# Kernel optimization log

Hardware: AMD Instinct MI355X
Metric: run time of the kernel (lower is better)

The kernel has to match this reference:

```python
import jax, jax.numpy as jnp
from jax import lax
import numpy as np

B, Z, Y, X = 2, 41, 400, 352   # KITTI-like sparse grid
N_TOTAL = 400000               # total active voxels (all batches)
C = 16                         # 16 * SCALING_RATIO channels in stage 1
K = 27                         # 3x3x3 kernel offsets
BN_EPS = 1e-3


def _build_rulebook(rng):
    """Random unique active voxels + [27,N] submanifold neighbor table (-1 = missing)."""
    per_b = N_TOTAL // B
    coords = []
    for b in range(B):
        flat = rng.choice(Z * Y * X, size=per_b, replace=False)
        z, r = np.divmod(flat, Y * X)
        y, x = np.divmod(r, X)
        coords.append(np.stack([np.full(per_b, b), z, y, x], axis=1))
    coords = np.concatenate(coords, 0).astype(np.int32)  # [N,4]
    # padded dense lookup: grid coord -> global voxel row, -1 if inactive
    lut = np.full((B, Z + 2, Y + 2, X + 2), -1, dtype=np.int32)
    lut[coords[:, 0], coords[:, 1] + 1, coords[:, 2] + 1, coords[:, 3] + 1] = np.arange(N_TOTAL, dtype=np.int32)
    offs = [(dz, dy, dx) for dz in (-1, 0, 1) for dy in (-1, 0, 1) for dx in (-1, 0, 1)]
    nbr = np.empty((K, N_TOTAL), dtype=np.int32)
    for k, (dz, dy, dx) in enumerate(offs):
        nbr[k] = lut[coords[:, 0], coords[:, 1] + 1 + dz, coords[:, 2] + 1 + dy, coords[:, 3] + 1 + dx]
    return nbr


def setup_inputs() -> dict:
    key = jax.random.key(0)
    kf, kw0, kw1, kg = jax.random.split(key, 4)
    rng = np.random.default_rng(0)
    nbr = jnp.asarray(_build_rulebook(rng))                      # [27, N] int32
    voxel_features = jax.random.normal(kf, (N_TOTAL, C), jnp.float32)
    w_in = jax.random.normal(kw0, (K, C, C), jnp.float32) * 0.05  # conv_input weight
    g_in = jnp.ones((C,), jnp.float32)
    b_in = jnp.zeros((C,), jnp.float32)
    # 2 SparseBasicBlocks x 2 convs each
    wb = jax.random.normal(kw1, (2, 2, K, C, C), jnp.float32) * 0.05
    gs = jnp.ones((2, 2, C), jnp.float32)
    bs = jnp.zeros((2, 2, C), jnp.float32)
    return {"voxel_features": voxel_features, "nbr": nbr, "w_in": w_in,
            "g_in": g_in, "b_in": b_in, "wb": wb, "gs": gs, "bs": bs}


def _subm_conv(feats, nbr, W):
    """Submanifold 3x3x3 conv: gather active neighbors, GEMM per offset, accumulate.
    feats [N,Cin], nbr [27,N] int32 (-1 = inactive), W [27,Cin,Cout] -> [N,Cout]."""
    out0 = jnp.zeros((feats.shape[0], W.shape[-1]), feats.dtype)
    def body(acc, kw):
        idx, Wk = kw
        valid = idx >= 0
        g = jnp.where(valid[:, None], feats[jnp.where(valid, idx, 0)], 0.0)
        return acc + g @ Wk, None
    acc, _ = lax.scan(body, out0, (nbr, W))
    return acc


def _bn(x, gamma, beta):
    # train-mode BatchNorm1d over voxel dim (biased var, eps=1e-3)
    m = x.mean(0)
    v = x.var(0)
    return (x - m) * lax.rsqrt(v + BN_EPS) * gamma + beta


def reference(voxel_features, nbr, w_in, g_in, b_in, wb, gs, bs):
    # conv_input: SubMConv3d -> BN -> ReLU
    x = jax.nn.relu(_bn(_subm_conv(voxel_features, nbr, w_in), g_in, b_in))
    # conv1: two SparseBasicBlocks sharing the 'subm1' rulebook
    for i in range(2):
        identity = x
        o = jax.nn.relu(_bn(_subm_conv(x, nbr, wb[i, 0]), gs[i, 0], bs[i, 0]))
        o = _bn(_subm_conv(o, nbr, wb[i, 1]), gs[i, 1], bs[i, 1])
        x = jax.nn.relu(o + identity)
    return x
```

## Files before the change

### kernel.cpp

```cpp
#include <hip/hip_runtime.h>

#define N_TOT  400000
#define NTILE  25000
#define NELEM  (N_TOT * 16)
#define CBLK   512
#define GSTRIDE (CBLK * 4)

typedef __attribute__((ext_vector_type(8))) short short8;
typedef __attribute__((ext_vector_type(4))) float f32x4;
typedef __attribute__((ext_vector_type(4))) unsigned short us4;

__device__ __forceinline__ unsigned short f2bf(float x) {
    unsigned int u = __float_as_uint(x);
    u += 0x7FFFu + ((u >> 16) & 1u);
    return (unsigned short)(u >> 16);
}
__device__ __forceinline__ float bf2f(unsigned short h) {
    return __uint_as_float(((unsigned int)h) << 16);
}

__global__ __launch_bounds__(64) void wfrag_k(const float* __restrict__ w_in,
                                              const float* __restrict__ wbs,
                                              unsigned short* __restrict__ wfrag,
                                              unsigned short* __restrict__ xb,
                                              unsigned short* __restrict__ ob) {
    if (blockIdx.x == 0 && threadIdx.x < 8) {
        us4 z = {0, 0, 0, 0};
        unsigned short* base = (threadIdx.x < 4) ? xb : ob;
        reinterpret_cast<us4*>(base + NELEM)[threadIdx.x & 3] = z;
    }
    int b = blockIdx.x;
    int L = b / 14, p = b % 14;
    int l = threadIdx.x;
    int g = l >> 4, col = l & 15;
    int k = 2 * p + (g >> 1);
    int cib = (g & 1) * 8;
    unsigned short v[8];
#pragma unroll
    for (int j = 0; j < 8; ++j) {
        float w = 0.f;
        if (k < 27) {
            int ci = cib + j;
            w = (L == 0) ? w_in[(k * 16 + ci) * 16 + col]
                         : wbs[(((L - 1) * 27 + k) * 16 + ci) * 16 + col];
        }
        v[j] = f2bf(w);
    }
    unsigned short* dst = wfrag + (size_t)(b * 64 + l) * 8;
#pragma unroll
    for (int j = 0; j < 8; ++j) dst[j] = v[j];
}

__global__ __launch_bounds__(256) void cvt_k(const float* __restrict__ in,
                                             unsigned short* __restrict__ out) {
    int i = (blockIdx.x * 256 + threadIdx.x) * 8;
    f32x4 a = *reinterpret_cast<const f32x4*>(in + i);
    f32x4 b = *reinterpret_cast<const f32x4*>(in + i + 4);
    short8 o = { (short)f2bf(a[0]), (short)f2bf(a[1]), (short)f2bf(a[2]), (short)f2bf(a[3]),
                 (short)f2bf(b[0]), (short)f2bf(b[1]), (short)f2bf(b[2]), (short)f2bf(b[3]) };
    *reinterpret_cast<short8*>(out + i) = o;
}

#define IDX(I, tt)                                                              \
  {                                                                             \
    const int vv = (tt) * 16;                                                   \
    _Pragma("unroll")                                                           \
    for (int p = 0; p < 14; ++p) {                                              \
      int k = 2 * p + ksel;                                                     \
      if (k == 13)      I[p] = vv + rc;                                         \
      else if (k < 27)  I[p] = nbr[(size_t)k * N_TOT + vv + rc];                \
      else              I[p] = -1;                                              \
    }                                                                           \
  }

#define GAT(A, I)                                                               \
  {                                                                             \
    _Pragma("unroll")                                                           \
    for (int p = 0; p < 14; ++p) {                                              \
      int ci = I[p] < 0 ? N_TOT : I[p];                                         \
      A[p] = *reinterpret_cast<const short8*>(feats + ((size_t)ci << 4) + half);\
    }                                                                           \
  }

#define CMP(A, tt)                                                              \
  {                                                                             \
    f32x4 acc = {0.f, 0.f, 0.f, 0.f};                                           \
    _Pragma("unroll")                                                           \
    for (int p = 0; p < 14; ++p) {                                              \
      short8 bf = *reinterpret_cast<const short8*>(&wlds[(p * 64 + lane) * 8]); \
      acc = __builtin_amdgcn_mfma_f32_16x16x32_bf16(A[p], bf, acc, 0, 0, 0);    \
    }                                                                           \
    const int vv = (tt) * 16;                                                   \
    _Pragma("unroll")                                                           \
    for (int i = 0; i < 4; ++i)                                                 \
      raw[(size_t)(vv + g * 4 + i) * 16 + rc] = f2bf(acc[i]);                   \
    s_acc += acc[0] + acc[1] + acc[2] + acc[3];                                 \
    q_acc += acc[0]*acc[0] + acc[1]*acc[1] + acc[2]*acc[2] + acc[3]*acc[3];     \
  }

__global__ __launch_bounds__(256, 2) void conv_k(const unsigned short* __restrict__ feats,
                                                 const int* __restrict__ nbr,
                                                 const unsigned short* __restrict__ wfrag,
                                                 unsigned short* __restrict__ raw,
                                                 float* __restrict__ partials) {
    __shared__ unsigned short wlds[14 * 64 * 8];
    __shared__ float red[128];

    {
        const f32x4* src = reinterpret_cast<const f32x4*>(wfrag);
        f32x4* dst = reinterpret_cast<f32x4*>(wlds);
        for (int j = threadIdx.x; j < 896; j += 256) dst[j] = src[j];
    }
    __syncthreads();

    const int lane = threadIdx.x & 63;
    const int wv   = threadIdx.x >> 6;
    const int g    = lane >> 4;
    const int rc   = lane & 15;
    const int half = (g & 1) * 8;
    const int ksel = g >> 1;

    float s_acc = 0.f, q_acc = 0.f;

    int I0[14], I1[14];
    short8 A0[14], A1[14];

    int t0 = blockIdx.x * 4 + wv;
    IDX(I0, t0);
    GAT(A0, I0);
    int t1 = t0 + GSTRIDE;
    if (t1 < NTILE) IDX(I1, t1);

    for (;;) {
        int t2 = t0 + 2 * GSTRIDE;
        if (t2 < NTILE) IDX(I0, t2);
        if (t1 < NTILE) GAT(A1, I1);
        __builtin_amdgcn_sched_barrier(0);
        CMP(A0, t0);
        if (t1 >= NTILE) break;

        int t3 = t1 + 2 * GSTRIDE;
        if (t3 < NTILE) IDX(I1, t3);
        if (t2 < NTILE) GAT(A0, I0);
        __builtin_amdgcn_sched_barrier(0);
        CMP(A1, t1);
        if (t2 >= NTILE) break;

        t0 = t2;
        t1 = t2 + GSTRIDE;
    }

    s_acc += __shfl_xor(s_acc, 16);  s_acc += __shfl_xor(s_acc, 32);
    q_acc += __shfl_xor(q_acc, 16);  q_acc += __shfl_xor(q_acc, 32);
    if (lane < 16) {
        red[wv * 32 + rc]      = s_acc;
        red[wv * 32 + 16 + rc] = q_acc;
    }
    __syncthreads();
    if (threadIdx.x < 32) {
        float v = red[threadIdx.x] + red[32 + threadIdx.x] +
                  red[64 + threadIdx.x] + red[96 + threadIdx.x];
        partials[(size_t)threadIdx.x * CBLK + blockIdx.x] = v;
    }
}

__global__ __launch_bounds__(256) void reduce_k(const float* __restrict__ partials,
                                                float* __restrict__ S) {
    int c = blockIdx.x;
    float s = 0.f;
    for (int i = threadIdx.x; i < CBLK; i += 256) s += partials[(size_t)c * CBLK + i];
    __shared__ float red[256];
    red[threadIdx.x] = s;
    __syncthreads();
#pragma unroll
    for (int off = 128; off > 0; off >>= 1) {
        if (threadIdx.x < off) red[threadIdx.x] += red[threadIdx.x + off];
        __syncthreads();
    }
    if (threadIdx.x == 0) S[c] = red[0];
}

__global__ __launch_bounds__(256) void apply_k(const unsigned short* __restrict__ raw,
                                               const float* __restrict__ S,
                                               const float* __restrict__ gamma,
                                               const float* __restrict__ beta,
                                               const unsigned short* residb,
                                               unsigned short* bfout,
                                               float* f32out) {
    int i = (blockIdx.x * 256 + threadIdx.x) * 8;
    int c0 = i & 8;
    short8 r8 = *reinterpret_cast<const short8*>(raw + i);
    float res[8] = {0, 0, 0, 0, 0, 0, 0, 0};
    if (residb) {
        short8 x8 = *reinterpret_cast<const short8*>(residb + i);
#pragma unroll
        for (int j = 0; j < 8; ++j) res[j] = bf2f((unsigned short)x8[j]);
    }
    const float inv = 1.0f / (float)N_TOT;
    float val[8];
#pragma unroll
    for (int j = 0; j < 8; ++j) {
        int c = c0 + j;
        float m   = S[c] * inv;
        float var = S[16 + c] * inv - m * m;
        float sc  = gamma[c] * rsqrtf(var + 1e-3f);
        float sh  = beta[c] - m * sc;
        val[j] = fmaxf(bf2f((unsigned short)r8[j]) * sc + sh + res[j], 0.f);
    }
    if (bfout) {
        short8 o = { (short)f2bf(val[0]), (short)f2bf(val[1]), (short)f2bf(val[2]), (short)f2bf(val[3]),
                     (short)f2bf(val[4]), (short)f2bf(val[5]), (short)f2bf(val[6]), (short)f2bf(val[7]) };
        *reinterpret_cast<short8*>(bfout + i) = o;
    }
    if (f32out) {
        f32x4 lo = { val[0], val[1], val[2], val[3] };
        f32x4 hi = { val[4], val[5], val[6], val[7] };
        *reinterpret_cast<f32x4*>(f32out + i)     = lo;
        *reinterpret_cast<f32x4*>(f32out + i + 4) = hi;
    }
}

extern "C" void kernel_launch(void* const* d_in, const int* in_sizes, int n_in,
                              void* d_out, int out_size, void* d_ws, size_t ws_size,
                              hipStream_t stream) {
    const float* vf   = (const float*)d_in[0];
    const int*   nbr  = (const int*)  d_in[1];
    const float* w_in = (const float*)d_in[2];
    const float* g_in = (const float*)d_in[3];
    const float* b_in = (const float*)d_in[4];
    const float* wbs  = (const float*)d_in[5];
    const float* gs   = (const float*)d_in[6];
    const float* bs   = (const float*)d_in[7];
    float* out = (float*)d_out;

    char* ws = (char*)d_ws;
    size_t off = 0;
    auto alloc = [&](size_t b) { char* p = ws + off; off += (b + 255) & ~(size_t)255; return p; };
    unsigned short* wfrag = (unsigned short*)alloc((size_t)5 * 14 * 64 * 8 * 2);
    unsigned short* xb    = (unsigned short*)alloc((size_t)(NELEM + 16) * 2);
    unsigned short* ob    = (unsigned short*)alloc((size_t)(NELEM + 16) * 2);
    unsigned short* rb    = (unsigned short*)alloc((size_t)NELEM * 2);
    float*          part  = (float*)alloc((size_t)32 * CBLK * 4);
    float*          S     = (float*)alloc(32 * 4);

    const int FR = 14 * 64 * 8;

    wfrag_k<<<70, 64, 0, stream>>>(w_in, wbs, wfrag, xb, ob);
    cvt_k<<<3125, 256, 0, stream>>>(vf, xb);

    conv_k<<<CBLK, 256, 0, stream>>>(xb, nbr, wfrag, rb, part);
    reduce_k<<<32, 256, 0, stream>>>(part, S);
    apply_k<<<3125, 256, 0, stream>>>(rb, S, g_in, b_in, nullptr, xb, nullptr);

    conv_k<<<CBLK, 256, 0, stream>>>(xb, nbr, wfrag + FR, rb, part);
    reduce_k<<<32, 256, 0, stream>>>(part, S);
    apply_k<<<3125, 256, 0, stream>>>(rb, S, gs + 0, bs + 0, nullptr, ob, nullptr);

    conv_k<<<CBLK, 256, 0, stream>>>(ob, nbr, wfrag + 2 * FR, rb, part);
    reduce_k<<<32, 256, 0, stream>>>(part, S);
    apply_k<<<3125, 256, 0, stream>>>(rb, S, gs + 16, bs + 16, xb, xb, nullptr);

    conv_k<<<CBLK, 256, 0, stream>>>(xb, nbr, wfrag + 3 * FR, rb, part);
    reduce_k<<<32, 256, 0, stream>>>(part, S);
    apply_k<<<3125, 256, 0, stream>>>(rb, S, gs + 32, bs + 32, nullptr, ob, nullptr);

    conv_k<<<CBLK, 256, 0, stream>>>(ob, nbr, wfrag + 4 * FR, rb, part);
    reduce_k<<<32, 256, 0, stream>>>(part, S);
    apply_k<<<3125, 256, 0, stream>>>(rb, S, gs + 48, bs + 48, xb, nullptr, out);
}
```

Baseline: 177.8 us.

## Deepen conv gather pipeline to three stages with predicated neighbor loads

The conv kernel's software pipeline goes from double to triple buffering, so index loads run three tiles ahead and feature gathers two tiles ahead of the MFMA compute. Neighbor-table loads are marked nontemporal, and missing neighbors are now zero-filled by a predicated load instead of reading a zero padding row. The zero-padding rows and their initialization are removed. The aim is to hide more gather latency, at the cost of more registers per thread, which may spill or lower occupancy under launch_bounds(256,2).

```diff
diff --git a/kernel.cpp b/kernel.cpp
--- a/kernel.cpp
+++ b/kernel.cpp
@@ -4,7 +4,7 @@
 #define NTILE  25000
 #define NELEM  (N_TOT * 16)
 #define CBLK   512
-#define GSTRIDE (CBLK * 4)
+#define GS     (CBLK * 4)
 
 typedef __attribute__((ext_vector_type(8))) short short8;
 typedef __attribute__((ext_vector_type(4))) float f32x4;
@@ -21,14 +21,7 @@
 
 __global__ __launch_bounds__(64) void wfrag_k(const float* __restrict__ w_in,
                                               const float* __restrict__ wbs,
-                                              unsigned short* __restrict__ wfrag,
-                                              unsigned short* __restrict__ xb,
-                                              unsigned short* __restrict__ ob) {
-    if (blockIdx.x == 0 && threadIdx.x < 8) {
-        us4 z = {0, 0, 0, 0};
-        unsigned short* base = (threadIdx.x < 4) ? xb : ob;
-        reinterpret_cast<us4*>(base + NELEM)[threadIdx.x & 3] = z;
-    }
+                                              unsigned short* __restrict__ wfrag) {
     int b = blockIdx.x;
     int L = b / 14, p = b % 14;
     int l = threadIdx.x;
@@ -68,7 +61,8 @@
     for (int p = 0; p < 14; ++p) {                                              \
       int k = 2 * p + ksel;                                                     \
       if (k == 13)      I[p] = vv + rc;                                         \
-      else if (k < 27)  I[p] = nbr[(size_t)k * N_TOT + vv + rc];                \
+      else if (k < 27)  I[p] = __builtin_nontemporal_load(                      \
+                                   &nbr[(size_t)k * N_TOT + vv + rc]);          \
       else              I[p] = -1;                                              \
     }                                                                           \
   }
@@ -77,8 +71,10 @@
   {                                                                             \
     _Pragma("unroll")                                                           \
     for (int p = 0; p < 14; ++p) {                                              \
-      int ci = I[p] < 0 ? N_TOT : I[p];                                         \
-      A[p] = *reinterpret_cast<const short8*>(feats + ((size_t)ci << 4) + half);\
+      short8 z = {0, 0, 0, 0, 0, 0, 0, 0};                                      \
+      A[p] = z;                                                                 \
+      if (I[p] >= 0)                                                            \
+        A[p] = *reinterpret_cast<const short8*>(feats + ((size_t)I[p] << 4) + half); \
     }                                                                           \
   }
 
@@ -96,6 +92,16 @@
       raw[(size_t)(vv + g * 4 + i) * 16 + rc] = f2bf(acc[i]);                   \
     s_acc += acc[0] + acc[1] + acc[2] + acc[3];                                 \
     q_acc += acc[0]*acc[0] + acc[1]*acc[1] + acc[2]*acc[2] + acc[3]*acc[3];     \
+  }
+
+#define ITER(Islot, Agat, Igat, Acmp)                                           \
+  {                                                                             \
+    if (tc + 3 * GS < NTILE) IDX(Islot, tc + 3 * GS);                           \
+    if (tc + 2 * GS < NTILE) GAT(Agat, Igat);                                   \
+    __builtin_amdgcn_sched_barrier(0);                                          \
+    CMP(Acmp, tc);                                                              \
+    tc += GS;                                                                   \
+    if (tc >= NTILE) break;                                                     \
   }
 
 __global__ __launch_bounds__(256, 2) void conv_k(const unsigned short* __restrict__ feats,
@@ -122,32 +128,22 @@
 
     float s_acc = 0.f, q_acc = 0.f;
 
-    int I0[14], I1[14];
-    short8 A0[14], A1[14];
-
-    int t0 = blockIdx.x * 4 + wv;
+    int I0[14], I1[14], I2[14];
+    short8 A0[14], A1[14], A2[14];
+
+    const int t0 = blockIdx.x * 4 + wv;
+    int tc = t0;
+
     IDX(I0, t0);
+    if (t0 + GS     < NTILE) IDX(I1, t0 + GS);
+    if (t0 + 2 * GS < NTILE) IDX(I2, t0 + 2 * GS);
     GAT(A0, I0);
-    int t1 = t0 + GSTRIDE;
-    if (t1 < NTILE) IDX(I1, t1);
+    if (t0 + GS < NTILE) { GAT(A1, I1); }
 
     for (;;) {
-        int t2 = t0 + 2 * GSTRIDE;
-        if (t2 < NTILE) IDX(I0, t2);
-        if (t1 < NTILE) GAT(A1, I1);
-        __builtin_amdgcn_sched_barrier(0);
-        CMP(A0, t0);
-        if (t1 >= NTILE) break;
-
-        int t3 = t1 + 2 * GSTRIDE;
-        if (t3 < NTILE) IDX(I1, t3);
-        if (t2 < NTILE) GAT(A0, I0);
-        __builtin_amdgcn_sched_barrier(0);
-        CMP(A1, t1);
-        if (t2 >= NTILE) break;
-
-        t0 = t2;
-        t1 = t2 + GSTRIDE;
+        ITER(I0, A2, I2, A0);
+        ITER(I1, A0, I0, A1);
+        ITER(I2, A1, I1, A2);
     }
 
     s_acc += __shfl_xor(s_acc, 16);  s_acc += __shfl_xor(s_acc, 32);
@@ -237,15 +233,15 @@
     size_t off = 0;
     auto alloc = [&](size_t b) { char* p = ws + off; off += (b + 255) & ~(size_t)255; return p; };
     unsigned short* wfrag = (unsigned short*)alloc((size_t)5 * 14 * 64 * 8 * 2);
-    unsigned short* xb    = (unsigned short*)alloc((size_t)(NELEM + 16) * 2);
-    unsigned short* ob    = (unsigned short*)alloc((size_t)(NELEM + 16) * 2);
+    unsigned short* xb    = (unsigned short*)alloc((size_t)NELEM * 2);
+    unsigned short* ob    = (unsigned short*)alloc((size_t)NELEM * 2);
     unsigned short* rb    = (unsigned short*)alloc((size_t)NELEM * 2);
     float*          part  = (float*)alloc((size_t)32 * CBLK * 4);
     float*          S     = (float*)alloc(32 * 4);
 
     const int FR = 14 * 64 * 8;
 
-    wfrag_k<<<70, 64, 0, stream>>>(w_in, wbs, wfrag, xb, ob);
+    wfrag_k<<<70, 64, 0, stream>>>(w_in, wbs, wfrag);
     cvt_k<<<3125, 256, 0, stream>>>(vf, xb);
 
     conv_k<<<CBLK, 256, 0, stream>>>(xb, nbr, wfrag, rb, part);
```

Result: slower. 254.0 us (+42.9%).

## Precompute per-tile neighbor validity masks to skip gathers, index loads and empty MFMAs

Applied to the files above, without the earlier changes.

Adds a one-time pass that ballots neighbor validity per 16-voxel tile and offset pair into a compact bitmask descriptor, reused by all five convolutions. The conv kernel consults the mask to skip loading neighbor indices and feature rows for missing neighbors, and skips MFMAs for offset pairs with no valid lanes. This cuts the memory traffic of the sparse rulebook and gather in exchange for an extra kernel, descriptor reads and divergent branches; the zero padding row is removed.

```diff
diff --git a/kernel.cpp b/kernel.cpp
--- a/kernel.cpp
+++ b/kernel.cpp
@@ -4,11 +4,10 @@
 #define NTILE  25000
 #define NELEM  (N_TOT * 16)
 #define CBLK   512
-#define GSTRIDE (CBLK * 4)
+#define GS     (CBLK * 4)
 
 typedef __attribute__((ext_vector_type(8))) short short8;
 typedef __attribute__((ext_vector_type(4))) float f32x4;
-typedef __attribute__((ext_vector_type(4))) unsigned short us4;
 
 __device__ __forceinline__ unsigned short f2bf(float x) {
     unsigned int u = __float_as_uint(x);
@@ -21,14 +20,7 @@
 
 __global__ __launch_bounds__(64) void wfrag_k(const float* __restrict__ w_in,
                                               const float* __restrict__ wbs,
-                                              unsigned short* __restrict__ wfrag,
-                                              unsigned short* __restrict__ xb,
-                                              unsigned short* __restrict__ ob) {
-    if (blockIdx.x == 0 && threadIdx.x < 8) {
-        us4 z = {0, 0, 0, 0};
-        unsigned short* base = (threadIdx.x < 4) ? xb : ob;
-        reinterpret_cast<us4*>(base + NELEM)[threadIdx.x & 3] = z;
-    }
+                                              unsigned short* __restrict__ wfrag) {
     int b = blockIdx.x;
     int L = b / 14, p = b % 14;
     int l = threadIdx.x;
@@ -61,34 +53,69 @@
     *reinterpret_cast<short8*>(out + i) = o;
 }
 
+__global__ __launch_bounds__(256) void desc_k(const int* __restrict__ nbr,
+                                              unsigned int* __restrict__ dsc) {
+    const int lane = threadIdx.x & 63;
+    const int wv   = threadIdx.x >> 6;
+    const int t    = blockIdx.x * 4 + wv;
+    const int g    = lane >> 4;
+    const int rc   = lane & 15;
+    const int ksel = g >> 1;
+    const int vv   = t * 16;
+#pragma unroll
+    for (int p = 0; p < 14; ++p) {
+        int k = 2 * p + ksel;
+        bool valid;
+        if (k == 13)     valid = true;
+        else if (k < 27) valid = nbr[(size_t)k * N_TOT + vv + rc] >= 0;
+        else             valid = false;
+        unsigned long long b = __ballot(valid);
+        unsigned int mask = (unsigned int)(b & 0xFFFFull) |
+                            ((unsigned int)(b >> 16) & 0xFFFF0000u);
+        if (lane == 0) dsc[(size_t)t * 14 + p] = mask;
+    }
+}
+
 #define IDX(I, tt)                                                              \
   {                                                                             \
     const int vv = (tt) * 16;                                                   \
+    const unsigned int* dp = dsc + (size_t)(tt) * 14;                           \
     _Pragma("unroll")                                                           \
     for (int p = 0; p < 14; ++p) {                                              \
       int k = 2 * p + ksel;                                                     \
-      if (k == 13)      I[p] = vv + rc;                                         \
-      else if (k < 27)  I[p] = nbr[(size_t)k * N_TOT + vv + rc];                \
-      else              I[p] = -1;                                              \
+      int id = -1;                                                              \
+      if (k == 13) id = vv + rc;                                                \
+      else if (k < 27) {                                                        \
+        unsigned int d = dp[p];                                                 \
+        if ((d >> bit) & 1u) id = nbr[(size_t)k * N_TOT + vv + rc];             \
+      }                                                                         \
+      I[p] = id;                                                                \
     }                                                                           \
   }
 
-#define GAT(A, I)                                                               \
+#define GAT(A, NE, I)                                                           \
   {                                                                             \
+    NE = 0;                                                                     \
     _Pragma("unroll")                                                           \
     for (int p = 0; p < 14; ++p) {                                              \
-      int ci = I[p] < 0 ? N_TOT : I[p];                                         \
-      A[p] = *reinterpret_cast<const short8*>(feats + ((size_t)ci << 4) + half);\
+      short8 z = {0, 0, 0, 0, 0, 0, 0, 0};                                      \
+      A[p] = z;                                                                 \
+      bool vld = I[p] >= 0;                                                     \
+      if (vld)                                                                  \
+        A[p] = *reinterpret_cast<const short8*>(feats + ((size_t)I[p] << 4) + half); \
+      if (__ballot(vld) != 0ull) NE |= (1 << p);                                \
     }                                                                           \
   }
 
-#define CMP(A, tt)                                                              \
+#define CMP(A, NE, tt)                                                          \
   {                                                                             \
     f32x4 acc = {0.f, 0.f, 0.f, 0.f};                                           \
     _Pragma("unroll")                                                           \
     for (int p = 0; p < 14; ++p) {                                              \
-      short8 bf = *reinterpret_cast<const short8*>(&wlds[(p * 64 + lane) * 8]); \
-      acc = __builtin_amdgcn_mfma_f32_16x16x32_bf16(A[p], bf, acc, 0, 0, 0);    \
+      if (__builtin_amdgcn_readfirstlane((NE >> p) & 1)) {                      \
+        short8 bf = *reinterpret_cast<const short8*>(&wlds[(p * 64 + lane) * 8]); \
+        acc = __builtin_amdgcn_mfma_f32_16x16x32_bf16(A[p], bf, acc, 0, 0, 0);  \
+      }                                                                         \
     }                                                                           \
     const int vv = (tt) * 16;                                                   \
     _Pragma("unroll")                                                           \
@@ -100,6 +127,7 @@
 
 __global__ __launch_bounds__(256, 2) void conv_k(const unsigned short* __restrict__ feats,
                                                  const int* __restrict__ nbr,
+                                                 const unsigned int* __restrict__ dsc,
                                                  const unsigned short* __restrict__ wfrag,
                                                  unsigned short* __restrict__ raw,
                                                  float* __restrict__ partials) {
@@ -119,35 +147,37 @@
     const int rc   = lane & 15;
     const int half = (g & 1) * 8;
     const int ksel = g >> 1;
+    const int bit  = ksel * 16 + rc;
 
     float s_acc = 0.f, q_acc = 0.f;
 
     int I0[14], I1[14];
     short8 A0[14], A1[14];
+    int ne0 = 0, ne1 = 0;
 
     int t0 = blockIdx.x * 4 + wv;
     IDX(I0, t0);
-    GAT(A0, I0);
-    int t1 = t0 + GSTRIDE;
+    GAT(A0, ne0, I0);
+    int t1 = t0 + GS;
     if (t1 < NTILE) IDX(I1, t1);
 
     for (;;) {
-        int t2 = t0 + 2 * GSTRIDE;
+        int t2 = t0 + 2 * GS;
         if (t2 < NTILE) IDX(I0, t2);
-        if (t1 < NTILE) GAT(A1, I1);
+        if (t1 < NTILE) GAT(A1, ne1, I1);
         __builtin_amdgcn_sched_barrier(0);
-        CMP(A0, t0);
+        CMP(A0, ne0, t0);
         if (t1 >= NTILE) break;
 
-        int t3 = t1 + 2 * GSTRIDE;
+        int t3 = t1 + 2 * GS;
         if (t3 < NTILE) IDX(I1, t3);
-        if (t2 < NTILE) GAT(A0, I0);
+        if (t2 < NTILE) GAT(A0, ne0, I0);
         __builtin_amdgcn_sched_barrier(0);
-        CMP(A1, t1);
+        CMP(A1, ne1, t1);
         if (t2 >= NTILE) break;
 
         t0 = t2;
-        t1 = t2 + GSTRIDE;
+        t1 = t2 + GS;
     }
 
     s_acc += __shfl_xor(s_acc, 16);  s_acc += __shfl_xor(s_acc, 32);
@@ -237,34 +267,36 @@
     size_t off = 0;
     auto alloc = [&](size_t b) { char* p = ws + off; off += (b + 255) & ~(size_t)255; return p; };
     unsigned short* wfrag = (unsigned short*)alloc((size_t)5 * 14 * 64 * 8 * 2);
-    unsigned short* xb    = (unsigned short*)alloc((size_t)(NELEM + 16) * 2);
-    unsigned short* ob    = (unsigned short*)alloc((size_t)(NELEM + 16) * 2);
+    unsigned short* xb    = (unsigned short*)alloc((size_t)NELEM * 2);
+    unsigned short* ob    = (unsigned short*)alloc((size_t)NELEM * 2);
     unsigned short* rb    = (unsigned short*)alloc((size_t)NELEM * 2);
+    unsigned int*   dsc   = (unsigned int*)alloc((size_t)NTILE * 14 * 4);
     float*          part  = (float*)alloc((size_t)32 * CBLK * 4);
     float*          S     = (float*)alloc(32 * 4);
 
     const int FR = 14 * 64 * 8;
 
-    wfrag_k<<<70, 64, 0, stream>>>(w_in, wbs, wfrag, xb, ob);
+    wfrag_k<<<70, 64, 0, stream>>>(w_in, wbs, wfrag);
     cvt_k<<<3125, 256, 0, stream>>>(vf, xb);
-
-    conv_k<<<CBLK, 256, 0, stream>>>(xb, nbr, wfrag, rb, part);
+    desc_k<<<6250, 256, 0, stream>>>(nbr, dsc);
+
+    conv_k<<<CBLK, 256, 0, stream>>>(xb, nbr, dsc, wfrag, rb, part);
     reduce_k<<<32, 256, 0, stream>>>(part, S);
     apply_k<<<3125, 256, 0, stream>>>(rb, S, g_in, b_in, nullptr, xb, nullptr);
 
-    conv_k<<<CBLK, 256, 0, stream>>>(xb, nbr, wfrag + FR, rb, part);
+    conv_k<<<CBLK, 256, 0, stream>>>(xb, nbr, dsc, wfrag + FR, rb, part);
     reduce_k<<<32, 256, 0, stream>>>(part, S);
     apply_k<<<3125, 256, 0, stream>>>(rb, S, gs + 0, bs + 0, nullptr, ob, nullptr);
 
-    conv_k<<<CBLK, 256, 0, stream>>>(ob, nbr, wfrag + 2 * FR, rb, part);
+    conv_k<<<CBLK, 256, 0, stream>>>(ob, nbr, dsc, wfrag + 2 * FR, rb, part);
     reduce_k<<<32, 256, 0, stream>>>(part, S);
     apply_k<<<3125, 256, 0, stream>>>(rb, S, gs + 16, bs + 16, xb, xb, nullptr);
 
-    conv_k<<<CBLK, 256, 0, stream>>>(xb, nbr, wfrag + 3 * FR, rb, part);
+    conv_k<<<CBLK, 256, 0, stream>>>(xb, nbr, dsc, wfrag + 3 * FR, rb, part);
     reduce_k<<<32, 256, 0, stream>>>(part, S);
     apply_k<<<3125, 256, 0, stream>>>(rb, S, gs + 32, bs + 32, nullptr, ob, nullptr);
 
-    conv_k<<<CBLK, 256, 0, stream>>>(ob, nbr, wfrag + 4 * FR, rb, part);
+    conv_k<<<CBLK, 256, 0, stream>>>(ob, nbr, dsc, wfrag + 4 * FR, rb, part);
     reduce_k<<<32, 256, 0, stream>>>(part, S);
     apply_k<<<3125, 256, 0, stream>>>(rb, S, gs + 48, bs + 48, xb, nullptr, out);
 }
```

New measurement: 448.7 us. 2.52x slower.

## Compact neighbor rulebook into per-tile masks and packed index lists

Applied to the files above, without the earlier changes.

Adds a one-time build kernel that converts the dense 27xN neighbor table into per-tile headers (26-bit validity mask per voxel plus prefix offset) and a packed list of valid neighbor indices. Each conv then decodes indices via popcount instead of reading 27 int32 per voxel, cutting index memory traffic across five convs. It also splits the MFMA accumulation into two independent chains to shorten the dependency chain. The cost is an extra preprocessing kernel and extra workspace, and invalid slots still issue a load from the compact array.

```diff
diff --git a/kernel.cpp b/kernel.cpp
--- a/kernel.cpp
+++ b/kernel.cpp
@@ -4,7 +4,7 @@
 #define NTILE  25000
 #define NELEM  (N_TOT * 16)
 #define CBLK   512
-#define GSTRIDE (CBLK * 4)
+#define GS     (CBLK * 4)
 
 typedef __attribute__((ext_vector_type(8))) short short8;
 typedef __attribute__((ext_vector_type(4))) float f32x4;
@@ -51,6 +51,44 @@
     for (int j = 0; j < 8; ++j) dst[j] = v[j];
 }
 
+__global__ __launch_bounds__(256) void build_k(const int* __restrict__ nbr,
+                                               int* __restrict__ thdr,
+                                               int* __restrict__ cidx) {
+    int tid = threadIdx.x;
+    int lane16 = tid & 15;
+    int t = blockIdx.x * 16 + (tid >> 4);
+    if (t >= NTILE) return;
+    int v = t * 16 + lane16;
+    unsigned mask = 0;
+    int vals[26];
+#pragma unroll
+    for (int k = 0; k < 27; ++k) {
+        if (k == 13) continue;
+        int slot = k < 13 ? k : k - 1;
+        int in_v = nbr[(size_t)k * N_TOT + v];
+        vals[slot] = in_v;
+        if (in_v >= 0) mask |= (1u << k);
+    }
+    int cnt = __popc(mask);
+    int pref = cnt;
+#pragma unroll
+    for (int d = 1; d < 16; d <<= 1) {
+        int n = __shfl_up(pref, d, 16);
+        if (lane16 >= d) pref += n;
+    }
+    int vo = pref - cnt;
+    int* hp = thdr + t * 32;
+    hp[lane16] = (int)mask;
+    *((unsigned char*)(hp + 16) + lane16) = (unsigned char)vo;
+    int pos = t * 64 + vo;
+#pragma unroll
+    for (int k = 0; k < 27; ++k) {
+        if (k == 13) continue;
+        int slot = k < 13 ? k : k - 1;
+        if (mask & (1u << k)) cidx[pos++] = vals[slot];
+    }
+}
+
 __global__ __launch_bounds__(256) void cvt_k(const float* __restrict__ in,
                                              unsigned short* __restrict__ out) {
     int i = (blockIdx.x * 256 + threadIdx.x) * 8;
@@ -61,15 +99,25 @@
     *reinterpret_cast<short8*>(out + i) = o;
 }
 
-#define IDX(I, tt)                                                              \
+#define IDXH(Hm, Hv, tt)                                                        \
   {                                                                             \
-    const int vv = (tt) * 16;                                                   \
+    const char* hp = (const char*)thdr + ((size_t)(tt) << 7);                   \
+    Hm = *reinterpret_cast<const int*>(hp + (rc << 2));                         \
+    Hv = *(const unsigned char*)(hp + 64 + rc);                                 \
+  }
+
+#define IDXD(I, Hm, Hv, tt)                                                     \
+  {                                                                             \
+    int cbase = ((tt) << 6) + Hv;                                               \
     _Pragma("unroll")                                                           \
     for (int p = 0; p < 14; ++p) {                                              \
       int k = 2 * p + ksel;                                                     \
-      if (k == 13)      I[p] = vv + rc;                                         \
-      else if (k < 27)  I[p] = nbr[(size_t)k * N_TOT + vv + rc];                \
-      else              I[p] = -1;                                              \
+      if (k == 13) I[p] = ((tt) << 4) + rc;                                     \
+      else if (k < 27) {                                                        \
+        unsigned below = ((unsigned)Hm) & ((kb << (2 * p)) - 1u);               \
+        int tmp = cidx[cbase + __popc(below)];                                  \
+        I[p] = ((Hm >> k) & 1) ? tmp : -1;                                      \
+      } else I[p] = -1;                                                         \
     }                                                                           \
   }
 
@@ -84,12 +132,16 @@
 
 #define CMP(A, tt)                                                              \
   {                                                                             \
-    f32x4 acc = {0.f, 0.f, 0.f, 0.f};                                           \
+    f32x4 ac0 = {0.f, 0.f, 0.f, 0.f};                                           \
+    f32x4 ac1 = {0.f, 0.f, 0.f, 0.f};                                           \
     _Pragma("unroll")                                                           \
-    for (int p = 0; p < 14; ++p) {                                              \
-      short8 bf = *reinterpret_cast<const short8*>(&wlds[(p * 64 + lane) * 8]); \
-      acc = __builtin_amdgcn_mfma_f32_16x16x32_bf16(A[p], bf, acc, 0, 0, 0);    \
+    for (int p = 0; p < 14; p += 2) {                                           \
+      short8 b0 = *reinterpret_cast<const short8*>(&wlds[(p * 64 + lane) * 8]); \
+      short8 b1 = *reinterpret_cast<const short8*>(&wlds[((p + 1) * 64 + lane) * 8]); \
+      ac0 = __builtin_amdgcn_mfma_f32_16x16x32_bf16(A[p],     b0, ac0, 0, 0, 0);\
+      ac1 = __builtin_amdgcn_mfma_f32_16x16x32_bf16(A[p + 1], b1, ac1, 0, 0, 0);\
     }                                                                           \
+    f32x4 acc = ac0 + ac1;                                                      \
     const int vv = (tt) * 16;                                                   \
     _Pragma("unroll")                                                           \
     for (int i = 0; i < 4; ++i)                                                 \
@@ -99,7 +151,8 @@
   }
 
 __global__ __launch_bounds__(256, 2) void conv_k(const unsigned short* __restrict__ feats,
-                                                 const int* __restrict__ nbr,
+                                                 const int* __restrict__ thdr,
+                                                 const int* __restrict__ cidx,
                                                  const unsigned short* __restrict__ wfrag,
                                                  unsigned short* __restrict__ raw,
                                                  float* __restrict__ partials) {
@@ -119,35 +172,39 @@
     const int rc   = lane & 15;
     const int half = (g & 1) * 8;
     const int ksel = g >> 1;
+    const unsigned kb = 1u << ksel;
 
     float s_acc = 0.f, q_acc = 0.f;
 
-    int I0[14], I1[14];
-    short8 A0[14], A1[14];
-
-    int t0 = blockIdx.x * 4 + wv;
-    IDX(I0, t0);
-    GAT(A0, I0);
-    int t1 = t0 + GSTRIDE;
-    if (t1 < NTILE) IDX(I1, t1);
+    int Ham, Hav, Hbm, Hbv;
+    int Ia[14], Ib[14];
+    short8 Aa[14], Ab[14];
+
+    int t  = blockIdx.x * 4 + wv;
+    int t1 = t + GS, t2 = t + 2 * GS;
+    IDXH(Ham, Hav, t);
+    IDXD(Ia, Ham, Hav, t);
+    GAT(Aa, Ia);
+    if (t1 < NTILE) { IDXH(Hbm, Hbv, t1); IDXD(Ib, Hbm, Hbv, t1); }
+    if (t2 < NTILE) IDXH(Ham, Hav, t2);
 
     for (;;) {
-        int t2 = t0 + 2 * GSTRIDE;
-        if (t2 < NTILE) IDX(I0, t2);
-        if (t1 < NTILE) GAT(A1, I1);
+        int t3 = t + 3 * GS;
+        if (t3 < NTILE) IDXH(Hbm, Hbv, t3);
+        if (t2 < NTILE) IDXD(Ia, Ham, Hav, t2);
+        if (t1 < NTILE) GAT(Ab, Ib);
         __builtin_amdgcn_sched_barrier(0);
-        CMP(A0, t0);
+        CMP(Aa, t);
         if (t1 >= NTILE) break;
-
-        int t3 = t1 + 2 * GSTRIDE;
-        if (t3 < NTILE) IDX(I1, t3);
-        if (t2 < NTILE) GAT(A0, I0);
+        t = t1; t1 = t + GS; t2 = t + 2 * GS; t3 = t + 3 * GS;
+
+        if (t3 < NTILE) IDXH(Ham, Hav, t3);
+        if (t2 < NTILE) IDXD(Ib, Hbm, Hbv, t2);
+        if (t1 < NTILE) GAT(Aa, Ia);
         __builtin_amdgcn_sched_barrier(0);
-        CMP(A1, t1);
-        if (t2 >= NTILE) break;
-
-        t0 = t2;
-        t1 = t2 + GSTRIDE;
+        CMP(Ab, t);
+        if (t1 >= NTILE) break;
+        t = t1; t1 = t + GS; t2 = t + 2 * GS;
     }
 
     s_acc += __shfl_xor(s_acc, 16);  s_acc += __shfl_xor(s_acc, 32);
@@ -240,31 +297,34 @@
     unsigned short* xb    = (unsigned short*)alloc((size_t)(NELEM + 16) * 2);
     unsigned short* ob    = (unsigned short*)alloc((size_t)(NELEM + 16) * 2);
     unsigned short* rb    = (unsigned short*)alloc((size_t)NELEM * 2);
+    int*            thdr  = (int*)alloc((size_t)NTILE * 128);
+    int*            cidx  = (int*)alloc(((size_t)NTILE * 64 + 64) * 4);
     float*          part  = (float*)alloc((size_t)32 * CBLK * 4);
     float*          S     = (float*)alloc(32 * 4);
 
     const int FR = 14 * 64 * 8;
 
     wfrag_k<<<70, 64, 0, stream>>>(w_in, wbs, wfrag, xb, ob);
+    build_k<<<1563, 256, 0, stream>>>(nbr, thdr, cidx);
     cvt_k<<<3125, 256, 0, stream>>>(vf, xb);
 
-    conv_k<<<CBLK, 256, 0, stream>>>(xb, nbr, wfrag, rb, part);
+    conv_k<<<CBLK, 256, 0, stream>>>(xb, thdr, cidx, wfrag, rb, part);
     reduce_k<<<32, 256, 0, stream>>>(part, S);
     apply_k<<<3125, 256, 0, stream>>>(rb, S, g_in, b_in, nullptr, xb, nullptr);
 
-    conv_k<<<CBLK, 256, 0, stream>>>(xb, nbr, wfrag + FR, rb, part);
+    conv_k<<<CBLK, 256, 0, stream>>>(xb, thdr, cidx, wfrag + FR, rb, part);
     reduce_k<<<32, 256, 0, stream>>>(part, S);
     apply_k<<<3125, 256, 0, stream>>>(rb, S, gs + 0, bs + 0, nullptr, ob, nullptr);
 
-    conv_k<<<CBLK, 256, 0, stream>>>(ob, nbr, wfrag + 2 * FR, rb, part);
+    conv_k<<<CBLK, 256, 0, stream>>>(ob, thdr, cidx, wfrag + 2 * FR, rb, part);
     reduce_k<<<32, 256, 0, stream>>>(part, S);
     apply_k<<<3125, 256, 0, stream>>>(rb, S, gs + 16, bs + 16, xb, xb, nullptr);
 
-    conv_k<<<CBLK, 256, 0, stream>>>(xb, nbr, wfrag + 3 * FR, rb, part);
+    conv_k<<<CBLK, 256, 0, stream>>>(xb, thdr, cidx, wfrag + 3 * FR, rb, part);
     reduce_k<<<32, 256, 0, stream>>>(part, S);
     apply_k<<<3125, 256, 0, stream>>>(rb, S, gs + 32, bs + 32, nullptr, ob, nullptr);
 
-    conv_k<<<CBLK, 256, 0, stream>>>(ob, nbr, wfrag + 4 * FR, rb, part);
+    conv_k<<<CBLK, 256, 0, stream>>>(ob, thdr, cidx, wfrag + 4 * FR, rb, part);
     reduce_k<<<32, 256, 0, stream>>>(part, S);
     apply_k<<<3125, 256, 0, stream>>>(rb, S, gs + 48, bs + 48, xb, nullptr, out);
 }
```

New measurement: 237.7 us. +33.7%, slower.
